# Performance work log

Measured on AMD Instinct MI355X. Metric: run time of the kernel, lower is better.

The kernel has to match this reference:

```python
import jax, jax.numpy as jnp
import numpy as np

LN_EPS = 1e-12


def setup_inputs() -> dict:
    key = jax.random.key(0)
    ks = jax.random.split(key, 6)
    B, S, H = 32, 512, 768
    P, K = 76, 64
    V, E = 50257, 768
    return {
        "sequence_data": jax.random.normal(ks[0], (B, S, H), dtype=jnp.float32),
        "masked_positions": jax.random.randint(ks[1], (B, P), 0, S, dtype=jnp.int64),
        "candidate_sets": jax.random.randint(ks[2], (B, P, K), 0, V, dtype=jnp.int64),
        "embedding_table": jax.random.normal(ks[3], (V, E), dtype=jnp.float32) * 0.02,
        "dense_w": jax.random.normal(ks[4], (H, E), dtype=jnp.float32) * (1.0 / np.sqrt(H)),
        "dense_b": jnp.zeros((E,), dtype=jnp.float32),
        "ln_gamma": jnp.ones((E,), dtype=jnp.float32),
        "ln_beta": jnp.zeros((E,), dtype=jnp.float32),
    }


def reference(sequence_data, masked_positions, candidate_sets, embedding_table,
              dense_w, dense_b, ln_gamma, ln_beta):
    # Gather masked positions: [B, P, H]
    gathered = jnp.take_along_axis(
        sequence_data, masked_positions[:, :, None], axis=1)
    # Dense (no activation), then LayerNorm (eps=1e-12)
    lm = jnp.einsum('bph,he->bpe', gathered, dense_w) + dense_b
    mu = jnp.mean(lm, axis=-1, keepdims=True)
    var = jnp.mean(jnp.square(lm - mu), axis=-1, keepdims=True)
    lm = (lm - mu) * jax.lax.rsqrt(var + LN_EPS) * ln_gamma + ln_beta
    # Candidate embedding gather: [B, P, K, E]
    cand = embedding_table[candidate_sets]
    # Inner products -> logits [B, P, K]
    logits = jnp.einsum('bpe,bpke->bpk', lm, cand)
    return logits
```

## Files before the change

kernel.cpp:

```cpp
#include <hip/hip_runtime.h>

typedef __attribute__((ext_vector_type(8))) short bf16x8;
typedef __attribute__((ext_vector_type(4))) float f32x4;

#define HH 768
#define EE 768
#define BB 32
#define SS 512
#define PP 76
#define KCAND 64
#define MM (BB * PP)

__device__ inline unsigned short f2bf(float f) {
    unsigned int u = __float_as_uint(f);
    u += 0x7fffu + ((u >> 16) & 1u);
    return (unsigned short)(u >> 16);
}

__global__ __launch_bounds__(256) void prep_w_kernel(
    const float* __restrict__ W, unsigned short* __restrict__ Wt) {
    __shared__ float tile[32][33];
    const int h0 = blockIdx.x * 32, e0 = blockIdx.y * 32;
    const int c = threadIdx.x & 31, r = threadIdx.x >> 5;
#pragma unroll
    for (int rr = r; rr < 32; rr += 8)
        tile[rr][c] = W[(size_t)(h0 + rr) * EE + e0 + c];
    __syncthreads();
#pragma unroll
    for (int rr = r; rr < 32; rr += 8)
        Wt[(size_t)(e0 + rr) * HH + h0 + c] = f2bf(tile[c][rr]);
}

__global__ __launch_bounds__(256) void gemm_kernel(
    const float* __restrict__ seq, const int* __restrict__ mpos,
    const unsigned short* __restrict__ Wt, float* __restrict__ lm) {
    __shared__ unsigned short Alds[64][72];
    __shared__ unsigned short Blds[64][72];
    const int bm = blockIdx.y, bn = blockIdx.x;
    const int tid = threadIdx.x;
    const int r = tid >> 2, q = tid & 3;

    const int gm = bm * 64 + r;
    const int b = gm / PP;
    const int p = gm - b * PP;
    const int ps = mpos[b * PP + p];
    const float* srow = seq + (size_t)(b * SS + ps) * HH;
    const unsigned short* wrow = Wt + (size_t)(bn * 64 + r) * HH;

    const int lane = tid & 63, wv = tid >> 6;
    const int wm = wv >> 1, wn = wv & 1;
    f32x4 acc[2][2] = {};

    for (int kk = 0; kk < HH; kk += 64) {
        __syncthreads();
#pragma unroll
        for (int j = 0; j < 4; ++j) {
            float4 v = *(const float4*)(srow + kk + q * 16 + j * 4);
            ushort4 s;
            s.x = f2bf(v.x); s.y = f2bf(v.y); s.z = f2bf(v.z); s.w = f2bf(v.w);
            *(ushort4*)&Alds[r][q * 16 + j * 4] = s;
        }
#pragma unroll
        for (int j = 0; j < 2; ++j) {
            int4 w = *(const int4*)(wrow + kk + q * 16 + j * 8);
            *(int4*)&Blds[r][q * 16 + j * 8] = w;
        }
        __syncthreads();
#pragma unroll
        for (int ks = 0; ks < 64; ks += 32) {
            bf16x8 af[2], bfr[2];
#pragma unroll
            for (int t = 0; t < 2; ++t)
                af[t] = *(const bf16x8*)&Alds[wm * 32 + t * 16 + (lane & 15)]
                                             [ks + (lane >> 4) * 8];
#pragma unroll
            for (int t = 0; t < 2; ++t)
                bfr[t] = *(const bf16x8*)&Blds[wn * 32 + t * 16 + (lane & 15)]
                                              [ks + (lane >> 4) * 8];
#pragma unroll
            for (int tm = 0; tm < 2; ++tm)
#pragma unroll
                for (int tn = 0; tn < 2; ++tn)
                    acc[tm][tn] = __builtin_amdgcn_mfma_f32_16x16x32_bf16(
                        af[tm], bfr[tn], acc[tm][tn], 0, 0, 0);
        }
    }
#pragma unroll
    for (int tm = 0; tm < 2; ++tm)
#pragma unroll
        for (int tn = 0; tn < 2; ++tn) {
            const int col = bn * 64 + wn * 32 + tn * 16 + (lane & 15);
            const int rbase = bm * 64 + wm * 32 + tm * 16 + (lane >> 4) * 4;
#pragma unroll
            for (int g = 0; g < 4; ++g)
                lm[(size_t)(rbase + g) * EE + col] = acc[tm][tn][g];
        }
}

__global__ __launch_bounds__(256) void logits_kernel(
    const float* __restrict__ lm, const float* __restrict__ bias,
    const float* __restrict__ gamma, const float* __restrict__ beta,
    const int* __restrict__ cand, const float* __restrict__ emb,
    float* __restrict__ out) {
    __shared__ float4 rowv4[192];
    __shared__ float reds[4], redq[4], stat[2];
    float* row = (float*)rowv4;
    const int bp = blockIdx.x;
    const int tid = threadIdx.x, lane = tid & 63, wv = tid >> 6;

    float s = 0.f, qq = 0.f;
    float v[3];
#pragma unroll
    for (int i = 0; i < 3; ++i) {
        const int idx = tid + i * 256;
        const float x = lm[(size_t)bp * EE + idx] + bias[idx];
        v[i] = x; s += x; qq += x * x;
    }
#pragma unroll
    for (int m = 32; m; m >>= 1) { s += __shfl_xor(s, m); qq += __shfl_xor(qq, m); }
    if (lane == 0) { reds[wv] = s; redq[wv] = qq; }
    __syncthreads();
    if (tid == 0) {
        const float S = reds[0] + reds[1] + reds[2] + reds[3];
        const float Q = redq[0] + redq[1] + redq[2] + redq[3];
        const float mu = S * (1.0f / 768.0f);
        const float var = Q * (1.0f / 768.0f) - mu * mu;
        stat[0] = mu; stat[1] = rsqrtf(var + 1e-12f);
    }
    __syncthreads();
    const float mu = stat[0], rstd = stat[1];
#pragma unroll
    for (int i = 0; i < 3; ++i) {
        const int idx = tid + i * 256;
        row[idx] = (v[i] - mu) * rstd * gamma[idx] + beta[idx];
    }
    __syncthreads();

    const float4 l0 = rowv4[lane], l1 = rowv4[lane + 64], l2 = rowv4[lane + 128];
    for (int k = wv; k < KCAND; k += 4) {
        const int cid = cand[bp * KCAND + k];
        const float4* er = (const float4*)(emb + (size_t)cid * EE);
        const float4 a = er[lane], b4 = er[lane + 64], c4 = er[lane + 128];
        float t = a.x * l0.x + a.y * l0.y + a.z * l0.z + a.w * l0.w
                + b4.x * l1.x + b4.y * l1.y + b4.z * l1.z + b4.w * l1.w
                + c4.x * l2.x + c4.y * l2.y + c4.z * l2.z + c4.w * l2.w;
#pragma unroll
        for (int m = 32; m; m >>= 1) t += __shfl_xor(t, m);
        if (lane == 0) out[bp * KCAND + k] = t;
    }
}

extern "C" void kernel_launch(void* const* d_in, const int* in_sizes, int n_in,
                              void* d_out, int out_size, void* d_ws, size_t ws_size,
                              hipStream_t stream) {
    const float* seq   = (const float*)d_in[0];
    const int*   mpos  = (const int*)d_in[1];
    const int*   cand  = (const int*)d_in[2];
    const float* emb   = (const float*)d_in[3];
    const float* W     = (const float*)d_in[4];
    const float* bias  = (const float*)d_in[5];
    const float* gamma = (const float*)d_in[6];
    const float* beta  = (const float*)d_in[7];
    float* out = (float*)d_out;

    unsigned short* Wt = (unsigned short*)d_ws;
    float* lm = (float*)((char*)d_ws + 1179648);

    prep_w_kernel<<<dim3(24, 24), 256, 0, stream>>>(W, Wt);
    gemm_kernel<<<dim3(12, 38), 256, 0, stream>>>(seq, mpos, Wt, lm);
    logits_kernel<<<MM, 256, 0, stream>>>(lm, bias, gamma, beta, cand, emb, out);
}
```

Baseline: 303.3 us.

## Pre-gather activations to bf16, widen GEMM K-tile, batch candidate embedding loads

```diff
diff --git a/kernel.cpp b/kernel.cpp
--- a/kernel.cpp
+++ b/kernel.cpp
@@ -17,66 +17,76 @@
     return (unsigned short)(u >> 16);
 }
 
-__global__ __launch_bounds__(256) void prep_w_kernel(
-    const float* __restrict__ W, unsigned short* __restrict__ Wt) {
-    __shared__ float tile[32][33];
-    const int h0 = blockIdx.x * 32, e0 = blockIdx.y * 32;
-    const int c = threadIdx.x & 31, r = threadIdx.x >> 5;
-#pragma unroll
-    for (int rr = r; rr < 32; rr += 8)
-        tile[rr][c] = W[(size_t)(h0 + rr) * EE + e0 + c];
-    __syncthreads();
-#pragma unroll
-    for (int rr = r; rr < 32; rr += 8)
-        Wt[(size_t)(e0 + rr) * HH + h0 + c] = f2bf(tile[c][rr]);
+__global__ __launch_bounds__(256) void prep_kernel(
+    const float* __restrict__ W, unsigned short* __restrict__ Wt,
+    const float* __restrict__ seq, const int* __restrict__ mpos,
+    unsigned short* __restrict__ Ag) {
+    const int bid = blockIdx.x;
+    if (bid < 576) {
+        __shared__ float tile[32][33];
+        const int h0 = (bid % 24) * 32, e0 = (bid / 24) * 32;
+        const int c = threadIdx.x & 31, r = threadIdx.x >> 5;
+#pragma unroll
+        for (int rr = r; rr < 32; rr += 8)
+            tile[rr][c] = W[(size_t)(h0 + rr) * EE + e0 + c];
+        __syncthreads();
+#pragma unroll
+        for (int rr = r; rr < 32; rr += 8)
+            Wt[(size_t)(e0 + rr) * HH + h0 + c] = f2bf(tile[c][rr]);
+    } else {
+        const int m0 = (bid - 576) * 8;
+        const int t = threadIdx.x;
+#pragma unroll
+        for (int rr = 0; rr < 8; ++rr) {
+            const int m = m0 + rr;
+            const int b = m / PP, p = m - b * PP;
+            const int ps = mpos[b * PP + p];
+            const float* srow = seq + (size_t)(b * SS + ps) * HH;
+            unsigned short* drow = Ag + (size_t)m * HH;
+#pragma unroll
+            for (int j = 0; j < 3; ++j) {
+                const int idx = t + j * 256;
+                drow[idx] = f2bf(srow[idx]);
+            }
+        }
+    }
 }
 
 __global__ __launch_bounds__(256) void gemm_kernel(
-    const float* __restrict__ seq, const int* __restrict__ mpos,
-    const unsigned short* __restrict__ Wt, float* __restrict__ lm) {
-    __shared__ unsigned short Alds[64][72];
-    __shared__ unsigned short Blds[64][72];
+    const unsigned short* __restrict__ Ag, const unsigned short* __restrict__ Wt,
+    float* __restrict__ lm) {
+    __shared__ unsigned short Alds[64][136];
+    __shared__ unsigned short Blds[64][136];
     const int bm = blockIdx.y, bn = blockIdx.x;
     const int tid = threadIdx.x;
-    const int r = tid >> 2, q = tid & 3;
-
-    const int gm = bm * 64 + r;
-    const int b = gm / PP;
-    const int p = gm - b * PP;
-    const int ps = mpos[b * PP + p];
-    const float* srow = seq + (size_t)(b * SS + ps) * HH;
-    const unsigned short* wrow = Wt + (size_t)(bn * 64 + r) * HH;
+    const int sr = tid >> 4;
+    const int sc = (tid & 15) * 8;
+    const unsigned short* abase = Ag + (size_t)(bm * 64) * HH;
+    const unsigned short* bbase = Wt + (size_t)(bn * 64) * HH;
 
     const int lane = tid & 63, wv = tid >> 6;
     const int wm = wv >> 1, wn = wv & 1;
+    const int fr = lane & 15, fq = (lane >> 4) * 8;
     f32x4 acc[2][2] = {};
 
-    for (int kk = 0; kk < HH; kk += 64) {
+    for (int kk = 0; kk < HH; kk += 128) {
         __syncthreads();
 #pragma unroll
-        for (int j = 0; j < 4; ++j) {
-            float4 v = *(const float4*)(srow + kk + q * 16 + j * 4);
-            ushort4 s;
-            s.x = f2bf(v.x); s.y = f2bf(v.y); s.z = f2bf(v.z); s.w = f2bf(v.w);
-            *(ushort4*)&Alds[r][q * 16 + j * 4] = s;
-        }
-#pragma unroll
-        for (int j = 0; j < 2; ++j) {
-            int4 w = *(const int4*)(wrow + kk + q * 16 + j * 8);
-            *(int4*)&Blds[r][q * 16 + j * 8] = w;
+        for (int rnd = 0; rnd < 4; ++rnd) {
+            const int row = sr + rnd * 16;
+            *(int4*)&Alds[row][sc] = *(const int4*)(abase + (size_t)row * HH + kk + sc);
+            *(int4*)&Blds[row][sc] = *(const int4*)(bbase + (size_t)row * HH + kk + sc);
         }
         __syncthreads();
 #pragma unroll
-        for (int ks = 0; ks < 64; ks += 32) {
+        for (int ks = 0; ks < 128; ks += 32) {
             bf16x8 af[2], bfr[2];
 #pragma unroll
             for (int t = 0; t < 2; ++t)
-                af[t] = *(const bf16x8*)&Alds[wm * 32 + t * 16 + (lane & 15)]
-                                             [ks + (lane >> 4) * 8];
+                af[t] = *(const bf16x8*)&Alds[wm * 32 + t * 16 + fr][ks + fq];
 #pragma unroll
             for (int t = 0; t < 2; ++t)
-                bfr[t] = *(const bf16x8*)&Blds[wn * 32 + t * 16 + (lane & 15)]
-                                              [ks + (lane >> 4) * 8];
+                bfr[t] = *(const bf16x8*)&Blds[wn * 32 + t * 16 + fr][ks + fq];
 #pragma unroll
             for (int tm = 0; tm < 2; ++tm)
 #pragma unroll
@@ -137,16 +147,35 @@
     __syncthreads();
 
     const float4 l0 = rowv4[lane], l1 = rowv4[lane + 64], l2 = rowv4[lane + 128];
-    for (int k = wv; k < KCAND; k += 4) {
-        const int cid = cand[bp * KCAND + k];
-        const float4* er = (const float4*)(emb + (size_t)cid * EE);
-        const float4 a = er[lane], b4 = er[lane + 64], c4 = er[lane + 128];
-        float t = a.x * l0.x + a.y * l0.y + a.z * l0.z + a.w * l0.w
-                + b4.x * l1.x + b4.y * l1.y + b4.z * l1.z + b4.w * l1.w
-                + c4.x * l2.x + c4.y * l2.y + c4.z * l2.z + c4.w * l2.w;
-#pragma unroll
-        for (int m = 32; m; m >>= 1) t += __shfl_xor(t, m);
-        if (lane == 0) out[bp * KCAND + k] = t;
+#pragma unroll
+    for (int it = 0; it < 4; ++it) {
+        const int k0 = wv * 16 + it * 4;
+        const float4* er[4];
+#pragma unroll
+        for (int c = 0; c < 4; ++c) {
+            const int cid = cand[bp * KCAND + k0 + c];
+            er[c] = (const float4*)(emb + (size_t)cid * EE);
+        }
+        float4 ra[4], rb[4], rc[4];
+#pragma unroll
+        for (int c = 0; c < 4; ++c) {
+            ra[c] = er[c][lane]; rb[c] = er[c][lane + 64]; rc[c] = er[c][lane + 128];
+        }
+        float t[4];
+#pragma unroll
+        for (int c = 0; c < 4; ++c)
+            t[c] = ra[c].x * l0.x + ra[c].y * l0.y + ra[c].z * l0.z + ra[c].w * l0.w
+                 + rb[c].x * l1.x + rb[c].y * l1.y + rb[c].z * l1.z + rb[c].w * l1.w
+                 + rc[c].x * l2.x + rc[c].y * l2.y + rc[c].z * l2.z + rc[c].w * l2.w;
+#pragma unroll
+        for (int m = 32; m; m >>= 1) {
+#pragma unroll
+            for (int c = 0; c < 4; ++c) t[c] += __shfl_xor(t[c], m);
+        }
+        if (lane == 0) {
+#pragma unroll
+            for (int c = 0; c < 4; ++c) out[bp * KCAND + k0 + c] = t[c];
+        }
     }
 }
 
@@ -164,9 +193,10 @@
     float* out = (float*)d_out;
 
     unsigned short* Wt = (unsigned short*)d_ws;
-    float* lm = (float*)((char*)d_ws + 1179648);
-
-    prep_w_kernel<<<dim3(24, 24), 256, 0, stream>>>(W, Wt);
-    gemm_kernel<<<dim3(12, 38), 256, 0, stream>>>(seq, mpos, Wt, lm);
+    unsigned short* Ag = (unsigned short*)((char*)d_ws + 1179648);
+    float* lm = (float*)((char*)d_ws + 1179648 + 3735552);
+
+    prep_kernel<<<880, 256, 0, stream>>>(W, Wt, seq, mpos, Ag);
+    gemm_kernel<<<dim3(12, 38), 256, 0, stream>>>(Ag, Wt, lm);
     logits_kernel<<<MM, 256, 0, stream>>>(lm, bias, gamma, beta, cand, emb, out);
 }
```

Result: faster. 292.2 us (-3.6%).
